# Kernel tuning notes

Hardware: AMD Instinct MI355X
Metric: run time of the kernel (lower is better)

The kernel has to match this reference:

```python
import jax, jax.numpy as jnp
import numpy as np
import math

H = 32       # num query heads
HKV = 8      # num kv heads
D = 64       # head_dim
ROPE_BASE = 10000.0


def rotate_half(x):
    x1, x2 = x[..., : x.shape[-1] // 2], x[..., x.shape[-1] // 2 :]
    return jnp.concatenate((-x2, x1), axis=-1)


def rope_cos_sin(T, dim, dtype):
    inv_freq = 1.0 / (ROPE_BASE ** (jnp.arange(0, dim, 2, dtype=jnp.float32) / dim))
    pos = jnp.arange(T, dtype=jnp.float32)
    freqs = pos[:, None] * inv_freq[None, :]          # [T, dim/2]
    emb = jnp.concatenate((freqs, freqs), axis=-1)    # [T, dim]
    return jnp.cos(emb).astype(dtype), jnp.sin(emb).astype(dtype)


def setup_inputs() -> dict:
    key = jax.random.key(0)
    ks = jax.random.split(key, 6)
    B, T, C = 2, 2048, 2048
    x = jax.random.normal(ks[0], (B, T, C), dtype=jnp.float32)
    mask = jnp.triu(jnp.ones((T, T), dtype=jnp.float32), k=1)  # 1 above diagonal (masked)
    s = 1.0 / math.sqrt(C)
    wq = jax.random.normal(ks[1], (C, C), dtype=jnp.float32) * s
    wk = jax.random.normal(ks[2], (HKV * D, C), dtype=jnp.float32) * s
    wv = jax.random.normal(ks[3], (HKV * D, C), dtype=jnp.float32) * s
    wc = jax.random.normal(ks[4], (C, C), dtype=jnp.float32) * s
    return {"x": x, "mask": mask, "wq": wq, "wk": wk, "wv": wv, "wc": wc}


def reference(x, mask, wq, wk, wv, wc):
    B, T, C = x.shape
    n_rep = H // HKV
    # projections (Linear: x @ W^T)
    q = (x @ wq.T).reshape(B, T, H, D).transpose(0, 2, 1, 3)      # [B,H,T,D]
    k = (x @ wk.T).reshape(B, T, HKV, D).transpose(0, 2, 1, 3)    # [B,HKV,T,D]
    v = (x @ wv.T).reshape(B, T, HKV, D).transpose(0, 2, 1, 3)
    # RoPE
    cos, sin = rope_cos_sin(T, D, x.dtype)                        # [T,D]
    cos, sin = cos[None, None], sin[None, None]                   # [1,1,T,D]
    q = q * cos + rotate_half(q) * sin
    k = k * cos + rotate_half(k) * sin
    # GQA expand kv heads
    k = jnp.repeat(k, n_rep, axis=1)                              # [B,H,T,D]
    v = jnp.repeat(v, n_rep, axis=1)
    # attention
    scores = jnp.einsum('bhqd,bhkd->bhqk', q, k) / math.sqrt(D)
    scores = scores + mask * (-1e9)
    attn = jax.nn.softmax(scores, axis=-1)
    y = jnp.einsum('bhqk,bhkd->bhqd', attn, v)                    # [B,H,T,D]
    y = y.transpose(0, 2, 1, 3).reshape(B, T, C)
    return y @ wc.T
```

## Files before the change

kernel.cpp:

```cpp
#include <hip/hip_runtime.h>
#include <hip/hip_bf16.h>
#include <math.h>

typedef unsigned short u16;
typedef short s16x8 __attribute__((ext_vector_type(8)));
typedef u16 u16x4 __attribute__((ext_vector_type(4)));
typedef __bf16 bf16x8_t __attribute__((ext_vector_type(8)));
typedef float f32x4 __attribute__((ext_vector_type(4)));

#define DEVI static __device__ __forceinline__

static constexpr int Bn = 2, Tn = 2048, Cn = 2048, Hn = 32, HKVn = 8, Dn = 64;
static constexpr int NCOL = Cn + 2 * HKVn * Dn;
#define QSCALE 0.18033688011f

#if __has_builtin(__builtin_amdgcn_exp2f)
#define EXP2(x) __builtin_amdgcn_exp2f(x)
#else
#define EXP2(x) exp2f(x)
#endif

DEVI u16 f2b(float f) {
  __hip_bfloat16 h = __float2bfloat16(f);
  return __builtin_bit_cast(u16, h);
}
DEVI float b2f(u16 u) {
  __hip_bfloat16 h = __builtin_bit_cast(__hip_bfloat16, u);
  return __bfloat162float(h);
}
DEVI bf16x8_t ld8(const u16* p) {
  s16x8 v = *reinterpret_cast<const s16x8*>(p);
  return __builtin_bit_cast(bf16x8_t, v);
}
DEVI f32x4 mfma16(bf16x8_t a, bf16x8_t b, f32x4 c) {
  return __builtin_amdgcn_mfma_f32_16x16x32_bf16(a, b, c, 0, 0, 0);
}
DEVI void async16(u16* lds_dst, const u16* gsrc) {
  __builtin_amdgcn_global_load_lds(
      (__attribute__((address_space(1))) void*)(gsrc),
      (__attribute__((address_space(3))) void*)(lds_dst), 16, 0, 0);
}

__global__ void cast_all(const float* __restrict__ x, const float* __restrict__ wq,
                         const float* __restrict__ wk, const float* __restrict__ wv,
                         const float* __restrict__ wc, u16* __restrict__ xb,
                         u16* __restrict__ wqkvb, u16* __restrict__ wcb) {
  constexpr int NX4 = 2097152, NWQ4 = 1048576, NWK4 = 262144;
  constexpr int TOT = NX4 + NWQ4 + 2 * NWK4 + NWQ4;
  const int stride = gridDim.x * blockDim.x;
  for (int i = blockIdx.x * blockDim.x + threadIdx.x; i < TOT; i += stride) {
    const float4* sv;
    u16x4* dv;
    if (i < NX4) {
      sv = (const float4*)x + i; dv = (u16x4*)xb + i;
    } else if (i < NX4 + NWQ4) {
      const int j = i - NX4;
      sv = (const float4*)wq + j; dv = (u16x4*)wqkvb + j;
    } else if (i < NX4 + NWQ4 + NWK4) {
      const int j = i - NX4 - NWQ4;
      sv = (const float4*)wk + j; dv = (u16x4*)wqkvb + NWQ4 + j;
    } else if (i < NX4 + NWQ4 + 2 * NWK4) {
      const int j = i - NX4 - NWQ4 - NWK4;
      sv = (const float4*)wv + j; dv = (u16x4*)wqkvb + NWQ4 + NWK4 + j;
    } else {
      const int j = i - NX4 - NWQ4 - 2 * NWK4;
      sv = (const float4*)wc + j; dv = (u16x4*)wcb + j;
    }
    const float4 v = *sv;
    u16x4 o = { f2b(v.x), f2b(v.y), f2b(v.z), f2b(v.w) };
    *dv = o;
  }
}

__global__ void rope_table_kernel(float* __restrict__ cs, float* __restrict__ sn) {
  int t = blockIdx.x;
  int d2 = threadIdx.x;
  float inv = powf(10000.0f, -(float)d2 / 32.0f);
  float fr = (float)t * inv;
  cs[t * 32 + d2] = cosf(fr);
  sn[t * 32 + d2] = sinf(fr);
}

__global__ __launch_bounds__(512, 2)
void gemm_qkv_rope256(const u16* __restrict__ A, const u16* __restrict__ Bm,
                      const float* __restrict__ cs, const float* __restrict__ sn,
                      u16* __restrict__ qo, u16* __restrict__ ko,
                      u16* __restrict__ vo, int K) {
  __shared__ u16 lds[2][4][8192];
  const int tid = threadIdx.x;
  const int mb = blockIdx.x * 256, nb = blockIdx.y * 256;
  const int lane = tid & 63, lr = lane & 15, lg = lane >> 4;
  const int w = tid >> 6, wm = w >> 2, wn = w & 3;
  const int nk = K >> 6;

  auto stage = [&](int buf, int kt) {
#pragma unroll
    for (int h = 0; h < 4; ++h)
#pragma unroll
      for (int i = 0; i < 2; ++i) {
        const int s = i * 512 + tid;
        const int row = s >> 3;
        const int c = (s & 7) ^ (row & 7);
        const u16* src = (h < 2)
            ? A + (size_t)(mb + h * 128 + row) * K + kt * 64 + c * 8
            : Bm + (size_t)(nb + (h - 2) * 128 + row) * K + kt * 64 + c * 8;
        async16(&lds[buf][h][s * 8], src);
      }
  };

  f32x4 acc[8][4] = {};
  stage(0, 0);
  stage(1, 1);

  for (int kt = 0; kt < nk; ++kt) {
    if (kt + 1 < nk) asm volatile("s_waitcnt vmcnt(8)" ::: "memory");
    else             asm volatile("s_waitcnt vmcnt(0)" ::: "memory");
    asm volatile("s_barrier" ::: "memory");
    const int buf = kt & 1;
    const u16* lA = &lds[buf][wm][0];
    const u16* lB = &lds[buf][2 + (wn >> 1)][0];
    const int brow = (wn & 1) * 64;
    bf16x8_t bfr[4][2];
#pragma unroll
    for (int n = 0; n < 4; ++n)
#pragma unroll
      for (int ks = 0; ks < 2; ++ks)
        bfr[n][ks] = ld8(lB + (brow + n * 16 + lr) * 64 +
                         (((ks * 4 + lg) ^ (lr & 7)) * 8));
#pragma unroll
    for (int p = 0; p < 4; ++p) {
      bf16x8_t af[2][2];
#pragma unroll
      for (int mi = 0; mi < 2; ++mi)
#pragma unroll
        for (int ks = 0; ks < 2; ++ks)
          af[mi][ks] = ld8(lA + ((p * 2 + mi) * 16 + lr) * 64 +
                           (((ks * 4 + lg) ^ (lr & 7)) * 8));
      __builtin_amdgcn_s_setprio(1);
#pragma unroll
      for (int mi = 0; mi < 2; ++mi)
#pragma unroll
        for (int n = 0; n < 4; ++n) {
          acc[p * 2 + mi][n] = mfma16(af[mi][0], bfr[n][0], acc[p * 2 + mi][n]);
          acc[p * 2 + mi][n] = mfma16(af[mi][1], bfr[n][1], acc[p * 2 + mi][n]);
        }
      __builtin_amdgcn_s_setprio(0);
    }
    asm volatile("s_barrier" ::: "memory");
    if (kt + 2 < nk) stage(buf, kt + 2);
  }
  __syncthreads();

  if (nb >= Cn + 512) {
#pragma unroll
    for (int m = 0; m < 8; ++m)
#pragma unroll
      for (int n = 0; n < 4; ++n) {
        const int row0 = mb + wm * 128 + m * 16 + lg * 4;
        const int col = nb + wn * 64 + n * 16 + lr;
        const int cc = col - Cn - 512;
        const int d = cc & 63, h = cc >> 6;
        const int b = row0 >> 11, t0 = row0 & 2047;
        u16x4 pk = { f2b(acc[m][n][0]), f2b(acc[m][n][1]),
                     f2b(acc[m][n][2]), f2b(acc[m][n][3]) };
        *reinterpret_cast<u16x4*>(
            vo + (((size_t)b * HKVn + h) * Dn + d) * Tn + t0) = pk;
      }
    return;
  }

  u16* tile = &lds[0][0][0];
#pragma unroll
  for (int m = 0; m < 8; ++m)
#pragma unroll
    for (int n = 0; n < 4; ++n) {
      const int colc = wn * 64 + n * 16 + lr;
      const int cc5 = colc >> 3;
#pragma unroll
      for (int r = 0; r < 4; ++r) {
        const int row = wm * 128 + m * 16 + lg * 4 + r;
        tile[row * 256 + ((cc5 ^ (row & 15)) << 3) + (colc & 7)] =
            f2b(acc[m][n][r]);
      }
    }
  __syncthreads();

  const bool isQ = (nb < Cn);
#pragma unroll
  for (int it = 0; it < 16; ++it) {
    const int unit = it * 512 + tid;
    const int tl = unit >> 5;
    const int ch = unit & 31;
    const int head = ch >> 3;
    const int c = ch & 7;
    const int sw = tl & 15;
    const s16x8 v0 = *reinterpret_cast<const s16x8*>(
        tile + tl * 256 + ((ch ^ sw) << 3));
    const s16x8 v1 = *reinterpret_cast<const s16x8*>(
        tile + tl * 256 + (((ch ^ 4) ^ sw) << 3));
    const int grow = mb + tl, b = grow >> 11, t = grow & 2047;
    const float4 c0 = *reinterpret_cast<const float4*>(cs + t * 32 + (c & 3) * 8);
    const float4 c1 = *reinterpret_cast<const float4*>(cs + t * 32 + (c & 3) * 8 + 4);
    const float4 s0 = *reinterpret_cast<const float4*>(sn + t * 32 + (c & 3) * 8);
    const float4 s1 = *reinterpret_cast<const float4*>(sn + t * 32 + (c & 3) * 8 + 4);
    const float cf[8] = { c0.x, c0.y, c0.z, c0.w, c1.x, c1.y, c1.z, c1.w };
    const float sf[8] = { s0.x, s0.y, s0.z, s0.w, s1.x, s1.y, s1.z, s1.w };
    const float sgn = (c < 4) ? -1.f : 1.f;
    const float scale = isQ ? QSCALE : 1.f;
    u16 outv[8];
#pragma unroll
    for (int e = 0; e < 8; ++e) {
      const float a0 = b2f((u16)v0[e]);
      const float a1 = b2f((u16)v1[e]);
      outv[e] = f2b((a0 * cf[e] + sgn * a1 * sf[e]) * scale);
    }
    u16* dst;
    if (isQ) {
      const int h = (nb >> 6) + head;
      dst = qo + (((size_t)b * Hn + h) * Tn + t) * Dn + c * 8;
    } else {
      const int h = ((nb - Cn) >> 6) + head;
      dst = ko + (((size_t)b * HKVn + h) * Tn + t) * Dn + c * 8;
    }
    *reinterpret_cast<s16x8*>(dst) = *reinterpret_cast<const s16x8*>(outv);
  }
}

__global__ __launch_bounds__(256)
void gemm_nt_f32(const u16* __restrict__ A, const u16* __restrict__ Bm,
                 float* __restrict__ Cm, int M, int N, int K) {
  constexpr int BM = 128, BK = 32;
  __shared__ u16 lds[2][2 * BM * BK];
  const int tid = threadIdx.x;
  const int mb = blockIdx.x * BM, nb = blockIdx.y * BM;
  const int lane = tid & 63;
  const int lr = lane & 15, lg = lane >> 4;
  const int w = tid >> 6, wm = w >> 1, wn = w & 1;
  const int nk = K >> 5;

  auto stage = [&](int buf, int kt) {
    const int r = tid >> 2;
    const int cx = ((tid & 3) ^ ((tid >> 3) & 3)) * 8;
    u16* lA = lds[buf];
    u16* lB = lds[buf] + BM * BK;
#pragma unroll
    for (int i = 0; i < 2; ++i) {
      async16(lA + i * 2048 + tid * 8, A + (size_t)(mb + i * 64 + r) * K + kt * BK + cx);
      async16(lB + i * 2048 + tid * 8, Bm + (size_t)(nb + i * 64 + r) * K + kt * BK + cx);
    }
  };

  const int rsw = (lr >> 1) & 3;
  f32x4 acc[4][4] = {};
  stage(0, 0);
  __syncthreads();
  int cur = 0;
  for (int kt = 0; kt < nk; ++kt) {
    if (kt + 1 < nk) stage(cur ^ 1, kt + 1);
    const u16* lA = lds[cur];
    const u16* lB = lds[cur] + BM * BK;
    bf16x8_t af[4], bfr[4];
#pragma unroll
    for (int i = 0; i < 4; ++i)
      af[i] = ld8(lA + (wm * 64 + i * 16 + lr) * BK + ((lg ^ rsw) * 8));
#pragma unroll
    for (int j = 0; j < 4; ++j)
      bfr[j] = ld8(lB + (wn * 64 + j * 16 + lr) * BK + ((lg ^ rsw) * 8));
#pragma unroll
    for (int i = 0; i < 4; ++i)
#pragma unroll
      for (int j = 0; j < 4; ++j)
        acc[i][j] = mfma16(af[i], bfr[j], acc[i][j]);
    __syncthreads();
    cur ^= 1;
  }
#pragma unroll
  for (int i = 0; i < 4; ++i)
#pragma unroll
    for (int j = 0; j < 4; ++j)
#pragma unroll
      for (int r = 0; r < 4; ++r) {
        const int row = mb + wm * 64 + i * 16 + lg * 4 + r;
        const int col = nb + wn * 64 + j * 16 + lr;
        Cm[(size_t)row * N + col] = acc[i][j][r];
      }
}

__global__ __launch_bounds__(256, 2)
void flash_kernel(const u16* __restrict__ q, const u16* __restrict__ k,
                  const u16* __restrict__ vt, u16* __restrict__ y) {
  __shared__ u16 kbuf[2][4096];
  __shared__ u16 vbuf[2][4096];
  __shared__ u16 plds[4][1024];
  const int tid = threadIdx.x;
  const int w = tid >> 6, lane = tid & 63, lr = lane & 15, lg = lane >> 4;
  const int bx = blockIdx.x;
  const int xb = 15 - (bx >> 6);
  const int bh = bx & 63;
  const int b = bh >> 5, h = bh & 31, hkv = h >> 2;
  const u16* kb_base = k + ((size_t)(b * HKVn + hkv)) * Tn * Dn;
  const u16* vb_base = vt + ((size_t)(b * HKVn + hkv)) * Dn * Tn;

  const int qb0 = xb * 128;
  const int ntiles = 2 * xb + 2;
  const int qw0 = qb0 + w * 32;
  const int qrow0 = qw0 + lr;

  const int slot0 = w * 128 + lane;
  const int slot1 = slot0 + 64;
  const int r0 = slot0 >> 3, c0 = (slot0 & 7) ^ (r0 & 7);
  const int r1 = slot1 >> 3, c1 = (slot1 & 7) ^ (r1 & 7);
  const u16* ksrc0 = kb_base + r0 * Dn + c0 * 8;
  const u16* ksrc1 = kb_base + r1 * Dn + c1 * 8;
  const u16* vsrc0 = vb_base + r0 * Tn + c0 * 8;
  const u16* vsrc1 = vb_base + r1 * Tn + c1 * 8;

  int off[4][2];
#pragma unroll
  for (int i = 0; i < 4; ++i)
#pragma unroll
    for (int ks = 0; ks < 2; ++ks)
      off[i][ks] = (i * 16 + lr) * 64 + (((ks * 4 + lg) ^ (lr & 7)) * 8);

  u16* pw = plds[w];
  const int swz = (lr & 7) * 8;

  auto stageKV = [&](int buf, int t) {
    const int ko = t * 64 * Dn;
    const int vo_ = t * 64;
    async16(&kbuf[buf][slot0 * 8], ksrc0 + ko);
    async16(&kbuf[buf][slot1 * 8], ksrc1 + ko);
    async16(&vbuf[buf][slot0 * 8], vsrc0 + vo_);
    async16(&vbuf[buf][slot1 * 8], vsrc1 + vo_);
  };

  bf16x8_t aq[2][2];
  {
    const u16* qp = q + (((size_t)(b * Hn + h)) * Tn + qw0 + lr) * Dn + lg * 8;
    aq[0][0] = ld8(qp);
    aq[0][1] = ld8(qp + 32);
    aq[1][0] = ld8(qp + 16 * Dn);
    aq[1][1] = ld8(qp + 16 * Dn + 32);
  }

  f32x4 acc[2][4] = {};
  float mrow[2] = { -3e38f, -3e38f };
  float lsum[2] = { 0.f, 0.f };

  stageKV(0, 0);
  stageKV(1, 1);

  for (int kb = 0; kb < ntiles; ++kb) {
    if (kb + 1 < ntiles) asm volatile("s_waitcnt vmcnt(4)" ::: "memory");
    else                 asm volatile("s_waitcnt vmcnt(0)" ::: "memory");
    asm volatile("s_barrier" ::: "memory");
    const int kp0 = kb * 64;
    if (kp0 <= qw0 + 31) {
      const u16* kl = kbuf[kb & 1];
      const u16* vl = vbuf[kb & 1];
      f32x4 sc[2][4] = {};
#pragma unroll
      for (int ks = 0; ks < 2; ++ks) {
        bf16x8_t kf0 = ld8(kl + off[0][ks]);
        bf16x8_t kf1 = ld8(kl + off[1][ks]);
        bf16x8_t kf2 = ld8(kl + off[2][ks]);
        bf16x8_t kf3 = ld8(kl + off[3][ks]);
#pragma unroll
        for (int rt = 0; rt < 2; ++rt) {
          sc[rt][0] = mfma16(kf0, aq[rt][ks], sc[rt][0]);
          sc[rt][1] = mfma16(kf1, aq[rt][ks], sc[rt][1]);
          sc[rt][2] = mfma16(kf2, aq[rt][ks], sc[rt][2]);
          sc[rt][3] = mfma16(kf3, aq[rt][ks], sc[rt][3]);
        }
      }
#pragma unroll
      for (int rt = 0; rt < 2; ++rt) {
        const int qrow = qrow0 + rt * 16;
        const bool needmask = (kp0 + 63) > (qw0 + rt * 16);
        if (needmask) {
#pragma unroll
          for (int kt = 0; kt < 4; ++kt) {
            const int kbase = kp0 + kt * 16 + lg * 4;
#pragma unroll
            for (int j = 0; j < 4; ++j)
              if ((kbase + j) > qrow) sc[rt][kt][j] = -3e38f;
          }
        }
        float m0 = fmaxf(fmaxf(sc[rt][0][0], sc[rt][0][1]),
                         fmaxf(sc[rt][0][2], sc[rt][0][3]));
        float m1 = fmaxf(fmaxf(sc[rt][1][0], sc[rt][1][1]),
                         fmaxf(sc[rt][1][2], sc[rt][1][3]));
        float m2 = fmaxf(fmaxf(sc[rt][2][0], sc[rt][2][1]),
                         fmaxf(sc[rt][2][2], sc[rt][2][3]));
        float m3 = fmaxf(fmaxf(sc[rt][3][0], sc[rt][3][1]),
                         fmaxf(sc[rt][3][2], sc[rt][3][3]));
        float pm = fmaxf(fmaxf(m0, m1), fmaxf(m2, m3));
        pm = fmaxf(pm, __shfl_xor(pm, 16, 64));
        pm = fmaxf(pm, __shfl_xor(pm, 32, 64));
        if (!__all(pm <= mrow[rt] + 8.0f)) {
          const float newm = fmaxf(mrow[rt], pm);
          const float sf = EXP2(mrow[rt] - newm);
          mrow[rt] = newm;
          lsum[rt] *= sf;
#pragma unroll
          for (int dt = 0; dt < 4; ++dt) acc[rt][dt] *= sf;
        }
        float tsum[4];
#pragma unroll
        for (int kt = 0; kt < 4; ++kt) {
#pragma unroll
          for (int j = 0; j < 4; ++j)
            sc[rt][kt][j] = EXP2(sc[rt][kt][j] - mrow[rt]);
          tsum[kt] = (sc[rt][kt][0] + sc[rt][kt][1]) +
                     (sc[rt][kt][2] + sc[rt][kt][3]);
        }
        float rs = (tsum[0] + tsum[1]) + (tsum[2] + tsum[3]);
        rs += __shfl_xor(rs, 16, 64);
        rs += __shfl_xor(rs, 32, 64);
        lsum[rt] += rs;
#pragma unroll
        for (int kt = 0; kt < 4; ++kt) {
          u16x4 pk = { f2b(sc[rt][kt][0]), f2b(sc[rt][kt][1]),
                       f2b(sc[rt][kt][2]), f2b(sc[rt][kt][3]) };
          *reinterpret_cast<u16x4*>(
              pw + lr * 64 + ((kt * 16 + lg * 4) ^ swz)) = pk;
        }
#pragma unroll
        for (int ks = 0; ks < 2; ++ks) {
          bf16x8_t pb = ld8(pw + lr * 64 + ((ks * 32 + lg * 8) ^ swz));
#pragma unroll
          for (int dt = 0; dt < 4; ++dt) {
            bf16x8_t vf = ld8(vl + off[dt][ks]);
            acc[rt][dt] = mfma16(vf, pb, acc[rt][dt]);
          }
        }
      }
    }
    asm volatile("s_barrier" ::: "memory");
    if (kb + 2 < ntiles) stageKV(kb & 1, kb + 2);
  }

  u16* scratch = &kbuf[0][0] + w * 2048;
#pragma unroll
  for (int rt = 0; rt < 2; ++rt) {
    float inv = 1.f / lsum[rt];
#pragma unroll
    for (int dt = 0; dt < 4; ++dt) {
      u16x4 pk = { f2b(acc[rt][dt][0] * inv), f2b(acc[rt][dt][1] * inv),
                   f2b(acc[rt][dt][2] * inv), f2b(acc[rt][dt][3] * inv) };
      *reinterpret_cast<u16x4*>(
          scratch + (rt * 16 + lr) * 64 + ((dt * 16 + lg * 4) ^ swz)) = pk;
    }
  }
#pragma unroll
  for (int it = 0; it < 4; ++it) {
    const int row = it * 8 + (lane >> 3);
    const int col = (lane & 7) * 8;
    s16x8 vv = *reinterpret_cast<const s16x8*>(
        scratch + row * 64 + (col ^ ((row & 7) * 8)));
    *reinterpret_cast<s16x8*>(
        y + ((size_t)b * Tn + qb0 + w * 32 + row) * Cn + h * 64 + col) = vv;
  }
}

extern "C" void kernel_launch(void* const* d_in, const int* in_sizes, int n_in,
                              void* d_out, int out_size, void* d_ws, size_t ws_size,
                              hipStream_t stream) {
  const float* x  = (const float*)d_in[0];
  const float* wq = (const float*)d_in[2];
  const float* wk = (const float*)d_in[3];
  const float* wv = (const float*)d_in[4];
  const float* wc = (const float*)d_in[5];
  float* out = (float*)d_out;
  char* ws = (char*)d_ws;

  const size_t NX   = (size_t)Bn * Tn * Cn;
  const size_t NWQ  = (size_t)Cn * Cn;
  const size_t NWK  = (size_t)HKVn * Dn * Cn;
  const size_t NQ   = (size_t)Bn * Hn * Tn * Dn;
  const size_t NKV  = (size_t)Bn * HKVn * Tn * Dn;

  size_t off = 0;
  u16* xb    = (u16*)(ws + off); off += NX * 2;
  u16* wqkvb = (u16*)(ws + off); off += (NWQ + 2 * NWK) * 2;
  u16* wcb   = (u16*)(ws + off); off += NWQ * 2;
  u16* qr    = (u16*)(ws + off); off += NQ * 2;
  u16* kr    = (u16*)(ws + off); off += NKV * 2;
  u16* vt    = (u16*)(ws + off); off += NKV * 2;
  float* cs  = (float*)(ws + off); off += (size_t)Tn * 32 * 4;
  float* sn  = (float*)(ws + off); off += (size_t)Tn * 32 * 4;

  u16* y = xb;

  cast_all<<<2048, 256, 0, stream>>>(x, wq, wk, wv, wc, xb, wqkvb, wcb);
  rope_table_kernel<<<Tn, 32, 0, stream>>>(cs, sn);

  gemm_qkv_rope256<<<dim3(16, 12), 512, 0, stream>>>(
      xb, wqkvb, cs, sn, qr, kr, vt, Cn);

  flash_kernel<<<dim3(1024), 256, 0, stream>>>(qr, kr, vt, y);

  gemm_nt_f32<<<dim3(32, 16), 256, 0, stream>>>(
      y, wcb, out, Bn * Tn, Cn, Cn);

  (void)in_sizes; (void)n_in; (void)out_size; (void)ws_size;
}
```

Measured before the change: 187.2 us.

## Retile QKV GEMM to 256x192 tiles and pair flash blocks by causal length

The QKV projection GEMM tile shrinks from 256x256 to 256x192, giving 256 blocks instead of 192 so the grid fills the 256 CUs better. The epilogue now handles tiles that straddle the Q/K/V column boundaries by deciding per fragment, and RoPE is applied per 8-column chunk. The flash kernel's block-to-query-tile mapping interleaves short and long causal rows (j and 15-j) to balance work across blocks. The trade-off is lower arithmetic intensity per tile and slightly more complex epilogue indexing.

```diff
diff --git a/kernel.cpp b/kernel.cpp
--- a/kernel.cpp
+++ b/kernel.cpp
@@ -86,47 +86,48 @@
                       const float* __restrict__ cs, const float* __restrict__ sn,
                       u16* __restrict__ qo, u16* __restrict__ ko,
                       u16* __restrict__ vo, int K) {
-  __shared__ u16 lds[2][4][8192];
+  __shared__ u16 lds[2][28672];
   const int tid = threadIdx.x;
-  const int mb = blockIdx.x * 256, nb = blockIdx.y * 256;
+  const int mb = blockIdx.x * 256, nb = blockIdx.y * 192;
   const int lane = tid & 63, lr = lane & 15, lg = lane >> 4;
   const int w = tid >> 6, wm = w >> 2, wn = w & 3;
   const int nk = K >> 6;
 
   auto stage = [&](int buf, int kt) {
 #pragma unroll
-    for (int h = 0; h < 4; ++h)
-#pragma unroll
-      for (int i = 0; i < 2; ++i) {
-        const int s = i * 512 + tid;
+    for (int h = 0; h < 7; ++h) {
+      if (h < 4) {
+        const int s = h * 512 + tid;
         const int row = s >> 3;
         const int c = (s & 7) ^ (row & 7);
-        const u16* src = (h < 2)
-            ? A + (size_t)(mb + h * 128 + row) * K + kt * 64 + c * 8
-            : Bm + (size_t)(nb + (h - 2) * 128 + row) * K + kt * 64 + c * 8;
-        async16(&lds[buf][h][s * 8], src);
+        async16(&lds[buf][s * 8], A + (size_t)(mb + row) * K + kt * 64 + c * 8);
+      } else {
+        const int s = (h - 4) * 512 + tid;
+        const int row = s >> 3;
+        const int c = (s & 7) ^ (row & 7);
+        async16(&lds[buf][16384 + s * 8],
+                Bm + (size_t)(nb + row) * K + kt * 64 + c * 8);
       }
+    }
   };
 
-  f32x4 acc[8][4] = {};
+  f32x4 acc[8][3] = {};
   stage(0, 0);
   stage(1, 1);
 
+  const int rsw = lr & 7;
   for (int kt = 0; kt < nk; ++kt) {
-    if (kt + 1 < nk) asm volatile("s_waitcnt vmcnt(8)" ::: "memory");
+    if (kt + 1 < nk) asm volatile("s_waitcnt vmcnt(7)" ::: "memory");
     else             asm volatile("s_waitcnt vmcnt(0)" ::: "memory");
     asm volatile("s_barrier" ::: "memory");
-    const int buf = kt & 1;
-    const u16* lA = &lds[buf][wm][0];
-    const u16* lB = &lds[buf][2 + (wn >> 1)][0];
-    const int brow = (wn & 1) * 64;
-    bf16x8_t bfr[4][2];
-#pragma unroll
-    for (int n = 0; n < 4; ++n)
+    const u16* base = lds[kt & 1];
+    bf16x8_t bfr[3][2];
+#pragma unroll
+    for (int n = 0; n < 3; ++n)
 #pragma unroll
       for (int ks = 0; ks < 2; ++ks)
-        bfr[n][ks] = ld8(lB + (brow + n * 16 + lr) * 64 +
-                         (((ks * 4 + lg) ^ (lr & 7)) * 8));
+        bfr[n][ks] = ld8(base + 16384 + (wn * 48 + n * 16 + lr) * 64 +
+                         (((ks * 4 + lg) ^ rsw) * 8));
 #pragma unroll
     for (int p = 0; p < 4; ++p) {
       bf16x8_t af[2][2];
@@ -134,70 +135,67 @@
       for (int mi = 0; mi < 2; ++mi)
 #pragma unroll
         for (int ks = 0; ks < 2; ++ks)
-          af[mi][ks] = ld8(lA + ((p * 2 + mi) * 16 + lr) * 64 +
-                           (((ks * 4 + lg) ^ (lr & 7)) * 8));
+          af[mi][ks] = ld8(base + (wm * 128 + (p * 2 + mi) * 16 + lr) * 64 +
+                           (((ks * 4 + lg) ^ rsw) * 8));
       __builtin_amdgcn_s_setprio(1);
 #pragma unroll
       for (int mi = 0; mi < 2; ++mi)
 #pragma unroll
-        for (int n = 0; n < 4; ++n) {
+        for (int n = 0; n < 3; ++n) {
           acc[p * 2 + mi][n] = mfma16(af[mi][0], bfr[n][0], acc[p * 2 + mi][n]);
           acc[p * 2 + mi][n] = mfma16(af[mi][1], bfr[n][1], acc[p * 2 + mi][n]);
         }
       __builtin_amdgcn_s_setprio(0);
     }
     asm volatile("s_barrier" ::: "memory");
-    if (kt + 2 < nk) stage(buf, kt + 2);
+    if (kt + 2 < nk) stage(kt & 1, kt + 2);
   }
   __syncthreads();
 
-  if (nb >= Cn + 512) {
-#pragma unroll
-    for (int m = 0; m < 8; ++m)
-#pragma unroll
-      for (int n = 0; n < 4; ++n) {
+  u16* tile = &lds[0][0];
+  bool anyQK = false;
+#pragma unroll
+  for (int m = 0; m < 8; ++m)
+#pragma unroll
+    for (int n = 0; n < 3; ++n) {
+      const int fragcol = nb + wn * 48 + n * 16;
+      if (fragcol >= Cn + 512) {
+        const int cc = fragcol + lr - Cn - 512;
+        const int d = cc & 63, h = cc >> 6;
         const int row0 = mb + wm * 128 + m * 16 + lg * 4;
-        const int col = nb + wn * 64 + n * 16 + lr;
-        const int cc = col - Cn - 512;
-        const int d = cc & 63, h = cc >> 6;
         const int b = row0 >> 11, t0 = row0 & 2047;
         u16x4 pk = { f2b(acc[m][n][0]), f2b(acc[m][n][1]),
                      f2b(acc[m][n][2]), f2b(acc[m][n][3]) };
         *reinterpret_cast<u16x4*>(
             vo + (((size_t)b * HKVn + h) * Dn + d) * Tn + t0) = pk;
+      } else {
+        anyQK = true;
+        const int colc = wn * 48 + n * 16 + lr;
+#pragma unroll
+        for (int r = 0; r < 4; ++r) {
+          const int row = wm * 128 + m * 16 + lg * 4 + r;
+          tile[row * 192 + (((colc >> 3) ^ (row & 7)) << 3) + (colc & 7)] =
+              f2b(acc[m][n][r]);
+        }
       }
-    return;
-  }
-
-  u16* tile = &lds[0][0][0];
-#pragma unroll
-  for (int m = 0; m < 8; ++m)
-#pragma unroll
-    for (int n = 0; n < 4; ++n) {
-      const int colc = wn * 64 + n * 16 + lr;
-      const int cc5 = colc >> 3;
-#pragma unroll
-      for (int r = 0; r < 4; ++r) {
-        const int row = wm * 128 + m * 16 + lg * 4 + r;
-        tile[row * 256 + ((cc5 ^ (row & 15)) << 3) + (colc & 7)] =
-            f2b(acc[m][n][r]);
-      }
-    }
+    }
+  if (nb >= Cn + 512) return;
+  (void)anyQK;
   __syncthreads();
 
-  const bool isQ = (nb < Cn);
-#pragma unroll
-  for (int it = 0; it < 16; ++it) {
+#pragma unroll
+  for (int it = 0; it < 12; ++it) {
     const int unit = it * 512 + tid;
-    const int tl = unit >> 5;
-    const int ch = unit & 31;
-    const int head = ch >> 3;
+    const int tl = unit / 24;
+    const int ch = unit - tl * 24;
+    const int gcol = nb + ch * 8;
+    if (gcol >= Cn + 512) continue;
     const int c = ch & 7;
-    const int sw = tl & 15;
+    const int sw = tl & 7;
     const s16x8 v0 = *reinterpret_cast<const s16x8*>(
-        tile + tl * 256 + ((ch ^ sw) << 3));
+        tile + tl * 192 + ((ch ^ sw) << 3));
     const s16x8 v1 = *reinterpret_cast<const s16x8*>(
-        tile + tl * 256 + (((ch ^ 4) ^ sw) << 3));
+        tile + tl * 192 + (((ch ^ 4) ^ sw) << 3));
     const int grow = mb + tl, b = grow >> 11, t = grow & 2047;
     const float4 c0 = *reinterpret_cast<const float4*>(cs + t * 32 + (c & 3) * 8);
     const float4 c1 = *reinterpret_cast<const float4*>(cs + t * 32 + (c & 3) * 8 + 4);
@@ -206,6 +204,7 @@
     const float cf[8] = { c0.x, c0.y, c0.z, c0.w, c1.x, c1.y, c1.z, c1.w };
     const float sf[8] = { s0.x, s0.y, s0.z, s0.w, s1.x, s1.y, s1.z, s1.w };
     const float sgn = (c < 4) ? -1.f : 1.f;
+    const bool isQ = (gcol < Cn);
     const float scale = isQ ? QSCALE : 1.f;
     u16 outv[8];
 #pragma unroll
@@ -216,10 +215,10 @@
     }
     u16* dst;
     if (isQ) {
-      const int h = (nb >> 6) + head;
+      const int h = gcol >> 6;
       dst = qo + (((size_t)b * Hn + h) * Tn + t) * Dn + c * 8;
     } else {
-      const int h = ((nb - Cn) >> 6) + head;
+      const int h = (gcol - Cn) >> 6;
       dst = ko + (((size_t)b * HKVn + h) * Tn + t) * Dn + c * 8;
     }
     *reinterpret_cast<s16x8*>(dst) = *reinterpret_cast<const s16x8*>(outv);
@@ -295,8 +294,10 @@
   const int tid = threadIdx.x;
   const int w = tid >> 6, lane = tid & 63, lr = lane & 15, lg = lane >> 4;
   const int bx = blockIdx.x;
-  const int xb = 15 - (bx >> 6);
-  const int bh = bx & 63;
+  const int pr = bx & 1, g = bx >> 1;
+  const int bh = g & 63;
+  const int j = (g >> 6) & 7;
+  const int xb = pr ? (15 - j) : j;
   const int b = bh >> 5, h = bh & 31, hkv = h >> 2;
   const u16* kb_base = k + ((size_t)(b * HKVn + hkv)) * Tn * Dn;
   const u16* vb_base = vt + ((size_t)(b * HKVn + hkv)) * Dn * Tn;
@@ -382,8 +383,8 @@
           for (int kt = 0; kt < 4; ++kt) {
             const int kbase = kp0 + kt * 16 + lg * 4;
 #pragma unroll
-            for (int j = 0; j < 4; ++j)
-              if ((kbase + j) > qrow) sc[rt][kt][j] = -3e38f;
+            for (int jj = 0; jj < 4; ++jj)
+              if ((kbase + jj) > qrow) sc[rt][kt][jj] = -3e38f;
           }
         }
         float m0 = fmaxf(fmaxf(sc[rt][0][0], sc[rt][0][1]),
@@ -409,8 +410,8 @@
 #pragma unroll
         for (int kt = 0; kt < 4; ++kt) {
 #pragma unroll
-          for (int j = 0; j < 4; ++j)
-            sc[rt][kt][j] = EXP2(sc[rt][kt][j] - mrow[rt]);
+          for (int jj = 0; jj < 4; ++jj)
+            sc[rt][kt][jj] = EXP2(sc[rt][kt][jj] - mrow[rt]);
           tsum[kt] = (sc[rt][kt][0] + sc[rt][kt][1]) +
                      (sc[rt][kt][2] + sc[rt][kt][3]);
         }
@@ -495,7 +496,7 @@
   cast_all<<<2048, 256, 0, stream>>>(x, wq, wk, wv, wc, xb, wqkvb, wcb);
   rope_table_kernel<<<Tn, 32, 0, stream>>>(cs, sn);
 
-  gemm_qkv_rope256<<<dim3(16, 12), 512, 0, stream>>>(
+  gemm_qkv_rope256<<<dim3(16, 16), 512, 0, stream>>>(
       xb, wqkvb, cs, sn, qr, kr, vt, Cn);
 
   flash_kernel<<<dim3(1024), 256, 0, stream>>>(qr, kr, vt, y);
```

Measured after the change: 217.6 us. 16.3% more time.
